# Performance work log

Hardware: AMD Instinct MI355X
Metric: run time of the kernel (lower is better)

Reference implementation:

```python
import jax, jax.numpy as jnp
import numpy as np
from jax import lax

B, T, I, O = 32, 4096, 16, 16


def setup_inputs() -> dict:
    key = jax.random.key(0)
    k1, k2, k3, k4 = jax.random.split(key, 4)
    u_in = jax.random.normal(k1, (B, T, I), dtype=jnp.float32)
    # parameters, initialized as in the torch module's __init__
    b_coeff = jax.random.normal(k2, (O, I, 2), dtype=jnp.float32) * 0.01
    rho = jax.random.normal(k3, (O, I, 1), dtype=jnp.float32) * 0.1
    psi = jax.random.normal(k4, (O, I, 1), dtype=jnp.float32) * 0.1
    return {"u_in": u_in, "b_coeff": b_coeff, "rho": rho, "psi": psi}


def _second_order_mimo(u_in, b_coeff, rho, psi):
    # stable parametrization of poles: r = |pole|, theta = angle
    r = jax.nn.sigmoid(rho)[..., 0]            # (O, I)
    theta = np.pi * jax.nn.sigmoid(psi)[..., 0]  # (O, I)
    a1 = -2.0 * r * jnp.cos(theta)             # (O, I)
    a2 = r * r                                  # (O, I)
    b0 = b_coeff[..., 0]                        # (O, I)
    b1 = b_coeff[..., 1]                        # (O, I)

    # FIR (moving-average) part, fully parallel over time:
    # x[b,t,o,i] = b0[o,i]*u[b,t,i] + b1[o,i]*u[b,t-1,i], zero initial condition
    u_prev = jnp.pad(u_in, ((0, 0), (1, 0), (0, 0)))[:, :-1, :]
    x = u_in[:, :, None, :] * b0 + u_prev[:, :, None, :] * b1  # (B, T, O, I)

    # AR (recursive) part: y[t] = x[t] - a1*y[t-1] - a2*y[t-2], per (o,i) pair
    x_t = jnp.moveaxis(x, 1, 0)  # (T, B, O, I)

    def step(carry, xt):
        y1, y2 = carry  # y[t-1], y[t-2], each (B, O, I)
        y = xt - a1 * y1 - a2 * y2
        return (y, y1), y

    y_init = jnp.zeros(x_t.shape[1:], x_t.dtype)
    _, ys = lax.scan(step, (y_init, y_init), x_t)  # (T, B, O, I)

    # sum per-input-channel filter responses -> (B, T, O)
    return jnp.moveaxis(ys.sum(axis=-1), 0, 1)


def reference(u_in, b_coeff, rho, psi):
    return _second_order_mimo(u_in, b_coeff, rho, psi)
```

## Files before the change

kernel.cpp:

```cpp
#include <hip/hip_runtime.h>
#include <math.h>

namespace {

constexpr int B = 32, T = 4096, I = 16, O = 16;

constexpr int C = 128;
constexpr int L = T / C;
constexpr int W = 24;
constexpr int PF = 8;
constexpr int FB = 8;

__device__ __forceinline__ void channel_params(const float* __restrict__ bc,
                                               const float* __restrict__ rho,
                                               const float* __restrict__ psi,
                                               int o, int i,
                                               float& b0, float& b1, float& a1, float& a2) {
    int oi = o * I + i;
    b0 = bc[oi * 2 + 0];
    b1 = bc[oi * 2 + 1];
    float r     = 1.0f / (1.0f + expf(-rho[oi]));
    float theta = 3.14159265358979323846f / (1.0f + expf(-psi[oi]));
    a1 = -2.0f * r * cosf(theta);
    a2 = r * r;
}

template <int NSTEP, int SKIP>
__device__ __forceinline__ void run_chain(const float* __restrict__ up,
        const float b0[4], const float b1[4], const float na1[4], const float na2[4],
        float uprev[4], float* __restrict__ op, bool writer) {
    static_assert((NSTEP - SKIP) % FB == 0, "stored steps multiple of flush block");
    float y1[4] = {0.f, 0.f, 0.f, 0.f};
    float y2[4] = {0.f, 0.f, 0.f, 0.f};
    float sv[FB];
    float4 buf[PF];
#pragma unroll
    for (int p = 0; p < PF; ++p) buf[p] = *(const float4*)(up + p * I);
#pragma unroll
    for (int t = 0; t < NSTEP; ++t) {
        float4 a = buf[t % PF];
        if (t + PF < NSTEP)
            buf[t % PF] = *(const float4*)(up + (t + PF) * I);
        float uc[4] = {a.x, a.y, a.z, a.w};
        float yv[4];
#pragma unroll
        for (int j = 0; j < 4; ++j) {
            float x = fmaf(b1[j], uprev[j], b0[j] * uc[j]);
            float y = fmaf(na2[j], y2[j], fmaf(na1[j], y1[j], x));
            y2[j] = y1[j]; y1[j] = y; uprev[j] = uc[j];
            yv[j] = y;
        }
        if (t >= SKIP) {
            int st = t - SKIP;
            sv[st % FB] = (yv[0] + yv[1]) + (yv[2] + yv[3]);
            if (st % FB == FB - 1) {
                int bt = st - (FB - 1);
#pragma unroll
                for (int m = 0; m < FB; ++m) {
                    float s = sv[m];
                    s += __shfl_xor(s, 1);
                    s += __shfl_xor(s, 2);
                    if (writer) op[(bt + m) * O] = s;
                }
            }
        }
    }
}

__global__ __launch_bounds__(256) void mimo_kernel(
        const float* __restrict__ u, const float* __restrict__ bc,
        const float* __restrict__ rho, const float* __restrict__ psi,
        float* __restrict__ out) {
    int g = blockIdx.x * blockDim.x + threadIdx.x;
    int q = g & 3, o = (g >> 2) & 15, b = (g >> 6) & 31, k = g >> 11;
    int i0 = q * 4;

    float b0[4], b1[4], na1[4], na2[4];
#pragma unroll
    for (int j = 0; j < 4; ++j) {
        float B0, B1, A1, A2;
        channel_params(bc, rho, psi, o, i0 + j, B0, B1, A1, A2);
        b0[j] = B0; b1[j] = B1; na1[j] = -A1; na2[j] = -A2;
    }

    int t0 = k * L;
    int start = (k == 0) ? 0 : (t0 - W);
    const float* up = u + ((size_t)b * T + start) * I + i0;

    float uprev[4];
    if (k == 0) {
#pragma unroll
        for (int j = 0; j < 4; ++j) uprev[j] = 0.0f;
    } else {
        float4 r0 = *(const float4*)(up - I);
        uprev[0] = r0.x; uprev[1] = r0.y; uprev[2] = r0.z; uprev[3] = r0.w;
    }

    float* op = out + ((size_t)b * T + t0) * O + o;
    bool writer = (q == 0);

    if (k == 0) run_chain<L, 0>(up, b0, b1, na1, na2, uprev, op, writer);
    else        run_chain<W + L, W>(up, b0, b1, na1, na2, uprev, op, writer);
}

}

extern "C" void kernel_launch(void* const* d_in, const int* in_sizes, int n_in,
                              void* d_out, int out_size, void* d_ws, size_t ws_size,
                              hipStream_t stream) {
    (void)in_sizes; (void)n_in; (void)out_size; (void)d_ws; (void)ws_size;
    const float* u   = (const float*)d_in[0];
    const float* bc  = (const float*)d_in[1];
    const float* rho = (const float*)d_in[2];
    const float* psi = (const float*)d_in[3];
    float* out = (float*)d_out;

    mimo_kernel<<<dim3((B * O * 4 * C) / 256), dim3(256), 0, stream>>>(
        u, bc, rho, psi, out);
}
```

Before: 79.11 us.

## Stage per-wavefront input window in LDS and process recurrence in blocks

Each wavefront shares the same batch and time chunk, so its 16 output channels used to issue redundant global loads of the same input rows. Now each wavefront cooperatively copies its input window, including the halo, into shared memory with coalesced float4 loads, and every lane reads its four input channels from LDS. The time loop is restructured into blocks of 8 steps: load 8 rows, run the recurrence, then shuffle-reduce and store. No barrier separates the LDS writes from the reads, so correctness relies on the 64 lanes of a wavefront executing together. The software prefetch ring is also dropped.

```diff
diff --git a/kernel.cpp b/kernel.cpp
--- a/kernel.cpp
+++ b/kernel.cpp
@@ -5,11 +5,12 @@
 
 constexpr int B = 32, T = 4096, I = 16, O = 16;
 
-constexpr int C = 128;
-constexpr int L = T / C;
-constexpr int W = 24;
-constexpr int PF = 8;
-constexpr int FB = 8;
+constexpr int C  = 128;
+constexpr int L  = T / C;
+constexpr int W  = 24;
+constexpr int NLMAX = 1 + W + L;
+constexpr int BS = 8;
+
 
 __device__ __forceinline__ void channel_params(const float* __restrict__ bc,
                                                const float* __restrict__ rho,
@@ -26,42 +27,40 @@
 }
 
 template <int NSTEP, int SKIP>
-__device__ __forceinline__ void run_chain(const float* __restrict__ up,
+__device__ __forceinline__ void run_chain(const float* __restrict__ ld,
         const float b0[4], const float b1[4], const float na1[4], const float na2[4],
         float uprev[4], float* __restrict__ op, bool writer) {
-    static_assert((NSTEP - SKIP) % FB == 0, "stored steps multiple of flush block");
+    static_assert(NSTEP % BS == 0 && SKIP % BS == 0, "blocks must align");
     float y1[4] = {0.f, 0.f, 0.f, 0.f};
     float y2[4] = {0.f, 0.f, 0.f, 0.f};
-    float sv[FB];
-    float4 buf[PF];
 #pragma unroll
-    for (int p = 0; p < PF; ++p) buf[p] = *(const float4*)(up + p * I);
+    for (int blk = 0; blk < NSTEP / BS; ++blk) {
+        float4 f[BS];
 #pragma unroll
-    for (int t = 0; t < NSTEP; ++t) {
-        float4 a = buf[t % PF];
-        if (t + PF < NSTEP)
-            buf[t % PF] = *(const float4*)(up + (t + PF) * I);
-        float uc[4] = {a.x, a.y, a.z, a.w};
-        float yv[4];
+        for (int m = 0; m < BS; ++m)
+            f[m] = *(const float4*)(ld + (blk * BS + m) * 16);
+        float sv[BS];
 #pragma unroll
-        for (int j = 0; j < 4; ++j) {
-            float x = fmaf(b1[j], uprev[j], b0[j] * uc[j]);
-            float y = fmaf(na2[j], y2[j], fmaf(na1[j], y1[j], x));
-            y2[j] = y1[j]; y1[j] = y; uprev[j] = uc[j];
-            yv[j] = y;
+        for (int m = 0; m < BS; ++m) {
+            float uc[4] = {f[m].x, f[m].y, f[m].z, f[m].w};
+            float yv[4];
+#pragma unroll
+            for (int j = 0; j < 4; ++j) {
+                float x = fmaf(b1[j], uprev[j], b0[j] * uc[j]);
+                float y = fmaf(na2[j], y2[j], fmaf(na1[j], y1[j], x));
+                y2[j] = y1[j]; y1[j] = y; uprev[j] = uc[j];
+                yv[j] = y;
+            }
+            sv[m] = (yv[0] + yv[1]) + (yv[2] + yv[3]);
         }
-        if (t >= SKIP) {
-            int st = t - SKIP;
-            sv[st % FB] = (yv[0] + yv[1]) + (yv[2] + yv[3]);
-            if (st % FB == FB - 1) {
-                int bt = st - (FB - 1);
+        if (blk * BS >= SKIP) {
+            int bt = blk * BS - SKIP;
 #pragma unroll
-                for (int m = 0; m < FB; ++m) {
-                    float s = sv[m];
-                    s += __shfl_xor(s, 1);
-                    s += __shfl_xor(s, 2);
-                    if (writer) op[(bt + m) * O] = s;
-                }
+            for (int m = 0; m < BS; ++m) {
+                float s = sv[m];
+                s += __shfl_xor(s, 1);
+                s += __shfl_xor(s, 2);
+                if (writer) op[(bt + m) * O] = s;
             }
         }
     }
@@ -71,36 +70,48 @@
         const float* __restrict__ u, const float* __restrict__ bc,
         const float* __restrict__ rho, const float* __restrict__ psi,
         float* __restrict__ out) {
+    __shared__ float lds[4 * NLMAX * 16];
     int g = blockIdx.x * blockDim.x + threadIdx.x;
     int q = g & 3, o = (g >> 2) & 15, b = (g >> 6) & 31, k = g >> 11;
-    int i0 = q * 4;
+    int lane = threadIdx.x & 63, wid = threadIdx.x >> 6;
+    float* wl = lds + wid * (NLMAX * 16);
+
+    int t0 = k * L;
+    int sline = (k == 0) ? 0 : (t0 - W - 1);
+    int nf = ((k == 0) ? L : NLMAX) * 4;
+    const float4* src = (const float4*)(u + ((size_t)b * T + sline) * I);
+    float4* dst = (float4*)wl;
+#pragma unroll
+    for (int r = 0; r < 4; ++r) {
+        int f = r * 64 + lane;
+        if (f < nf) dst[f] = src[f];
+    }
 
     float b0[4], b1[4], na1[4], na2[4];
 #pragma unroll
     for (int j = 0; j < 4; ++j) {
         float B0, B1, A1, A2;
-        channel_params(bc, rho, psi, o, i0 + j, B0, B1, A1, A2);
+        channel_params(bc, rho, psi, o, q * 4 + j, B0, B1, A1, A2);
         b0[j] = B0; b1[j] = B1; na1[j] = -A1; na2[j] = -A2;
     }
 
-    int t0 = k * L;
-    int start = (k == 0) ? 0 : (t0 - W);
-    const float* up = u + ((size_t)b * T + start) * I + i0;
-
     float uprev[4];
+    const float* ld;
     if (k == 0) {
 #pragma unroll
         for (int j = 0; j < 4; ++j) uprev[j] = 0.0f;
+        ld = wl + q * 4;
     } else {
-        float4 r0 = *(const float4*)(up - I);
+        float4 r0 = *(const float4*)(wl + q * 4);
         uprev[0] = r0.x; uprev[1] = r0.y; uprev[2] = r0.z; uprev[3] = r0.w;
+        ld = wl + 16 + q * 4;
     }
 
     float* op = out + ((size_t)b * T + t0) * O + o;
     bool writer = (q == 0);
 
-    if (k == 0) run_chain<L, 0>(up, b0, b1, na1, na2, uprev, op, writer);
-    else        run_chain<W + L, W>(up, b0, b1, na1, na2, uprev, op, writer);
+    if (k == 0) run_chain<L, 0>(ld, b0, b1, na1, na2, uprev, op, writer);
+    else        run_chain<W + L, W>(ld, b0, b1, na1, na2, uprev, op, writer);
 }
 
 }
```

Result: no change. 80.46 us (+1.7%).
